# Optimization experiments

Measured on AMD Instinct MI355X. Metric: run time of the kernel, lower is better.

Reference implementation:

```python
import jax, jax.numpy as jnp
import numpy as np

B, T_ENC, ENC_DIM = 32, 200, 256
T_DEC, DEC_OUT = 200, 80
HID = 256
PRENET1, PRENET2 = 256, 128


def _gru_cell(x, h, kernel, rec_kernel, bias):
    # Keras GRUCell, reset_after=True. bias: [2, 3*units] (input bias, recurrent bias)
    xz, xr, xh = jnp.split(x @ kernel + bias[0], 3, axis=-1)
    rz, rr, rh = jnp.split(h @ rec_kernel + bias[1], 3, axis=-1)
    z = jax.nn.sigmoid(xz + rz)
    r = jax.nn.sigmoid(xr + rr)
    hh = jnp.tanh(xh + r * rh)
    return z * h + (1.0 - z) * hh


def setup_inputs() -> dict:
    key = jax.random.key(0)
    ks = jax.random.split(key, 24)
    g = lambda k, shape: (jax.random.normal(k, shape, dtype=jnp.float32) / np.sqrt(shape[0] if len(shape) > 1 else 1.0))
    attn_in = PRENET2 + ENC_DIM  # prenet output concat prev attention
    return {
        "memory": jax.random.normal(ks[0], (B, T_ENC, ENC_DIM), dtype=jnp.float32),
        "dec_inputs": jax.random.normal(ks[1], (B, T_DEC, DEC_OUT), dtype=jnp.float32),
        # Prenet
        "fc1_w": g(ks[2], (DEC_OUT, PRENET1)), "fc1_b": jnp.zeros((PRENET1,), jnp.float32),
        "fc2_w": g(ks[3], (PRENET1, PRENET2)), "fc2_b": jnp.zeros((PRENET2,), jnp.float32),
        # Attention GRU cell
        "attn_k": g(ks[4], (attn_in, 3 * HID)), "attn_rk": g(ks[5], (HID, 3 * HID)),
        "attn_bias": jnp.zeros((2, 3 * HID), jnp.float32),
        # Bahdanau attention
        "W": g(ks[6], (ENC_DIM, ENC_DIM)), "U": g(ks[7], (HID, ENC_DIM)), "V": g(ks[8], (ENC_DIM, 1)),
        # Projection
        "proj_w": g(ks[9], (ENC_DIM + HID, HID)), "proj_b": jnp.zeros((HID,), jnp.float32),
        # Decoder GRU cells
        "rnn1_k": g(ks[10], (HID, 3 * HID)), "rnn1_rk": g(ks[11], (HID, 3 * HID)),
        "rnn1_bias": jnp.zeros((2, 3 * HID), jnp.float32),
        "rnn2_k": g(ks[12], (HID, 3 * HID)), "rnn2_rk": g(ks[13], (HID, 3 * HID)),
        "rnn2_bias": jnp.zeros((2, 3 * HID), jnp.float32),
        # Output projection
        "out_w": g(ks[14], (HID, DEC_OUT)), "out_b": jnp.zeros((DEC_OUT,), jnp.float32),
    }


def reference(memory, dec_inputs, fc1_w, fc1_b, fc2_w, fc2_b, attn_k, attn_rk,
              attn_bias, W, U, V, proj_w, proj_b, rnn1_k, rnn1_rk, rnn1_bias,
              rnn2_k, rnn2_rk, rnn2_bias, out_w, out_b):
    b = memory.shape[0]
    # W(values) is loop-invariant -> precompute (same math as in-step application)
    Wv = memory @ W  # [B, T_enc, ENC_DIM]

    def step(carry, x_t):
        attn, h_a, h1, h2 = carry
        # Prenet (Dropout is identity at inference)
        q = jax.nn.relu(x_t @ fc1_w + fc1_b)
        q = jax.nn.relu(q @ fc2_w + fc2_b)
        # Attention RNN
        h_a = _gru_cell(jnp.concatenate([q, attn], axis=-1), h_a, attn_k, attn_rk, attn_bias)
        # Bahdanau attention
        score = jnp.tanh(Wv + (h_a @ U)[:, None, :]) @ V           # [B, T_enc, 1]
        align = jax.nn.softmax(score, axis=1)                       # [B, T_enc, 1]
        attn = jnp.sum(align * memory, axis=1)                      # [B, ENC_DIM]
        # Projection + 2 decoder GRU cells with residual adds
        proj = jnp.concatenate([attn, h_a], axis=-1) @ proj_w + proj_b
        h1 = _gru_cell(proj, h1, rnn1_k, rnn1_rk, rnn1_bias)
        r1 = proj + h1
        h2 = _gru_cell(r1, h2, rnn2_k, rnn2_rk, rnn2_bias)
        r2 = r1 + h2
        out = r2 @ out_w + out_b
        return (attn, h_a, h1, h2), out

    init = (
        jnp.zeros((b, memory.shape[2]), memory.dtype),  # attention
        jnp.zeros((b, HID), memory.dtype),              # attn rnn state
        jnp.zeros((b, HID), memory.dtype),              # dec rnn1 state
        jnp.zeros((b, HID), memory.dtype),              # dec rnn2 state
    )
    xs = jnp.swapaxes(dec_inputs, 0, 1)  # [T_dec, B, DEC_OUT]
    _, ys = jax.lax.scan(step, init, xs)
    return jnp.swapaxes(ys, 0, 1)  # all_outputs: [B, T_dec, DEC_OUT]
```

## Files before the change

### kernel.cpp

```cpp
#include <hip/hip_runtime.h>
#include <math.h>


#define TENC 200
#define TDEC 200

typedef short bf16x8 __attribute__((ext_vector_type(8)));
typedef float f32x4  __attribute__((ext_vector_type(4)));

#define O_H1B   8192
#define O_H2B   (O_H1B + 16384)
#define O_R1B   (O_H2B + 16384)
#define ZERO_FLOATS (O_R1B + 16384)
#define O_HAS   57344
#define O_UHP   (O_HAS + 200*32*256)
#define O_NP    (O_UHP + 32*32*256)
#define O_ZP    (O_NP + 2*128*256)
#define O_PJ    (O_ZP + 256)
#define O_Q2    (O_PJ + 8192)
#define O_WV    (O_Q2 + 200*32*128)
#define O_R2S   (O_WV + 32*200*256)
#define O_IMG   (O_R2S + 200*32*256)

#define IMGA_OFF  0u
#define IMGC1_OFF 1327104u
#define IMGC2_OFF 1859584u
#define IMGD_OFF  2924544u

__device__ __forceinline__ float sigm(float x)  { return 1.0f / (1.0f + __expf(-x)); }
__device__ __forceinline__ float ftanh(float x) { return 1.0f - 2.0f / (1.0f + __expf(2.0f * x)); }

__device__ __forceinline__ unsigned short f2bf(float f) {
  union { float f; unsigned u; } v; v.f = f;
  return (unsigned short)((v.u + 0x7FFFu + ((v.u >> 16) & 1u)) >> 16);
}
__device__ __forceinline__ float bf2f(unsigned short h) {
  union { unsigned u; float f; } v; v.u = ((unsigned)h) << 16; return v.f;
}

__device__ __forceinline__ void pollwait(const unsigned* p, unsigned tgt, bool act) {
  for (;;) {
    bool ok = true;
    if (act) ok = (__hip_atomic_load(p, __ATOMIC_RELAXED, __HIP_MEMORY_SCOPE_AGENT) >= tgt);
    if (__syncthreads_and((int)ok)) break;
    __builtin_amdgcn_s_sleep(2);
  }
  __builtin_amdgcn_fence(__ATOMIC_ACQUIRE, "agent");
}
__device__ __forceinline__ void set_flag(unsigned* f, unsigned v) {
  __syncthreads();
  if (threadIdx.x == 0) {
    __builtin_amdgcn_fence(__ATOMIC_RELEASE, "agent");
    __hip_atomic_store(f, v, __ATOMIC_RELAXED, __HIP_MEMORY_SCOPE_AGENT);
  }
}

__global__ __launch_bounds__(256) void k_prep(
    const float* __restrict__ aK, const float* __restrict__ aRK,
    const float* __restrict__ Wp,
    const float* __restrict__ K1, const float* __restrict__ RK1,
    const float* __restrict__ K2, const float* __restrict__ RK2,
    unsigned short* __restrict__ img)
{
  int e = blockIdx.x * 256 + threadIdx.x;
  int id = blockIdx.y;
  float w = 0.f; size_t oh = 0, ol = 0;
  if (id == 0) {
    if (e >= 32*32*648) return;
    int k = e % 648, n = (e / 648) & 31, blk = e / (648*32);
    int u = blk*8 + (n & 7), g = n >> 3;
    if (k < 384) {
      w = (g==0) ? aK[(size_t)k*768+u] : (g==1) ? aK[(size_t)k*768+256+u]
        : (g==2) ? aK[(size_t)k*768+512+u] : 0.f;
    } else if (k < 640) {
      int kk = k - 384;
      w = (g==0) ? aRK[(size_t)kk*768+u] : (g==1) ? aRK[(size_t)kk*768+256+u]
        : (g==3) ? aRK[(size_t)kk*768+512+u] : 0.f;
    }
    size_t base = IMGA_OFF + (size_t)blk*2*32*648;
    oh = base + (size_t)n*648 + k; ol = oh + 32*648;
  } else if (id == 1) {
    if (e >= 32*16*520) return;
    int k = e % 520, n = (e / 520) & 15, blk = e / (520*16);
    if (n < 8 && k < 512) w = Wp[(size_t)k*256 + blk*8 + n];
    size_t base = IMGC1_OFF + (size_t)blk*2*16*520;
    oh = base + (size_t)n*520 + k; ol = oh + 16*520;
  } else {
    if (e >= 32*32*520) return;
    int k = e % 520, n = (e / 520) & 31, blk = e / (520*32);
    int u = blk*8 + (n & 7), g = n >> 3;
    const float* Kx = (id == 2) ? K1 : K2;
    const float* Rx = (id == 2) ? RK1 : RK2;
    if (k < 256) {
      w = (g==0) ? Kx[(size_t)k*768+u] : (g==1) ? Kx[(size_t)k*768+256+u]
        : (g==2) ? Kx[(size_t)k*768+512+u] : 0.f;
    } else if (k < 512) {
      int kk = k - 256;
      w = (g==0) ? Rx[(size_t)kk*768+u] : (g==1) ? Rx[(size_t)kk*768+256+u]
        : (g==3) ? Rx[(size_t)kk*768+512+u] : 0.f;
    }
    size_t base = ((id == 2) ? IMGC2_OFF : IMGD_OFF) + (size_t)blk*2*32*520;
    oh = base + (size_t)n*520 + k; ol = oh + 32*520;
  }
  unsigned short hi = f2bf(w);
  unsigned short lo = f2bf(w - bf2f(hi));
  img[oh] = hi; img[ol] = lo;
}

__global__ __launch_bounds__(256, 1) void k_scan6(
    const float* __restrict__ memg,
    const float* __restrict__ aB, const float* __restrict__ Uw,
    const float* __restrict__ Vw, const float* __restrict__ pb,
    const float* __restrict__ B1v, const float* __restrict__ B2v,
    float* __restrict__ ws)
{
  const int tid = threadIdx.x, bid = blockIdx.x;
  const int lane = tid & 63, wv = tid >> 6;
  unsigned* fl = (unsigned*)ws;
  float* fH1B = ws + O_H1B;  float* fH2B = ws + O_H2B;  float* fR1B = ws + O_R1B;
  float* fHAS = ws + O_HAS;  float* fUHP = ws + O_UHP;
  float* fNP  = ws + O_NP;   float* fZP  = ws + O_ZP;   float* fPJ = ws + O_PJ;
  float* fQ2  = ws + O_Q2;   float* fWV  = ws + O_WV;   float* fR2S = ws + O_R2S;
  const unsigned short* img = (const unsigned short*)(ws + O_IMG);

  __shared__ __align__(16) char smem[140544];

  if (bid < 32) {
    const int j = bid;
    unsigned* myflag = fl + (0 + j) * 32;
    unsigned short* sW = (unsigned short*)smem;
    unsigned short* sX = (unsigned short*)(smem + 82944);
    float* sU  = (float*)(smem + 124416);
    float* sOut= (float*)(smem + 132608);
    float* sHN = (float*)(smem + 137216);
    float* sHP = (float*)(smem + 138240);
    float* sB  = (float*)(smem + 139264);
    float* sZi = (float*)(smem + 139392);
    {
      const uint4* src = (const uint4*)(img + IMGA_OFF + (size_t)j*2*32*648);
      uint4* dst = (uint4*)sW;
      for (int i = tid; i < 82944/16; i += 256) dst[i] = src[i];
      for (int i = tid; i < 2048; i += 256)
        sU[i] = Uw[(size_t)(j*8 + (i >> 8))*256 + (i & 255)];
      if (tid < 8) {
        int u = j*8 + tid;
        sB[tid]      = aB[u]       + aB[768 + u];
        sB[8 + tid]  = aB[256 + u] + aB[1024 + u];
        sB[16 + tid] = aB[512 + u];
        sB[24 + tid] = aB[1280 + u];
      }
    }
    __syncthreads();
    for (int t = 0; t < TDEC; ++t) {
      for (int i = tid; i < 4096; i += 256) {
        int b = i >> 7, k = i & 127;
        sX[b*648 + k] = f2bf(fQ2[((size_t)t*32 + b)*128 + k]);
      }
      pollwait(fl + (32 + (tid & 127))*32, (unsigned)t, (t > 0) && (tid < 128));
      if (t > 0 && tid < 32) {
        int p = (t - 1) & 1;
        sZi[tid] = 1.0f / (fZP[p*128 + tid*4] + fZP[p*128 + tid*4 + 1] +
                           fZP[p*128 + tid*4 + 2] + fZP[p*128 + tid*4 + 3]);
      }
      __syncthreads();
      for (int i = tid; i < 8192; i += 256) {
        int b = i >> 8, d = i & 255; float v = 0.f;
        if (t > 0) {
          int p = (t - 1) & 1;
          const float* np = fNP + (size_t)p*32768 + (size_t)(b*4)*256 + d;
          v = (np[0] + np[256] + np[512] + np[768]) * sZi[b];
        }
        sX[b*648 + 128 + d] = f2bf(v);
      }
      for (int i = tid; i < 8192; i += 256) {
        int b = i >> 8, d = i & 255;
        float v = (t > 0) ? fHAS[((size_t)(t-1)*32 + b)*256 + d] : 0.f;
        sX[b*648 + 384 + d] = f2bf(v);
      }
      { int b = tid >> 3, ul = tid & 7;
        sHP[tid] = (t > 0) ? fHAS[((size_t)(t-1)*32 + b)*256 + j*8 + ul] : 0.f; }
      __syncthreads();
      {
        const int mt = wv >> 1, nt = wv & 1;
        f32x4 acc = {0.f, 0.f, 0.f, 0.f};
        const unsigned short* xr = sX + (size_t)(mt*16 + (lane&15))*648 + ((lane>>4)*8);
        const unsigned short* wh = sW + (size_t)(nt*16 + (lane&15))*648 + ((lane>>4)*8);
        const unsigned short* wl = wh + 32*648;
        for (int kt = 0; kt < 20; ++kt) {
          bf16x8 a  = *(const bf16x8*)(xr + kt*32);
          bf16x8 bh = *(const bf16x8*)(wh + kt*32);
          bf16x8 bl = *(const bf16x8*)(wl + kt*32);
          acc = __builtin_amdgcn_mfma_f32_16x16x32_bf16(a, bh, acc, 0, 0, 0);
          acc = __builtin_amdgcn_mfma_f32_16x16x32_bf16(a, bl, acc, 0, 0, 0);
        }
        int r0 = mt*16 + ((lane>>4)<<2), c = nt*16 + (lane&15);
        #pragma unroll
        for (int i2 = 0; i2 < 4; ++i2) sOut[(r0+i2)*36 + c] = acc[i2];
      }
      __syncthreads();
      { int b = tid >> 3, ul = tid & 7;
        float z = sigm(sOut[b*36 + ul] + sB[ul]);
        float r = sigm(sOut[b*36 + 8 + ul] + sB[8+ul]);
        float hh = ftanh(sOut[b*36 + 16 + ul] + sB[16+ul] + r*(sOut[b*36 + 24 + ul] + sB[24+ul]));
        float hn = z * sHP[tid] + (1.0f - z) * hh;
        sHN[tid] = hn;
        fHAS[((size_t)t*32 + b)*256 + j*8 + ul] = hn;
      }
      __syncthreads();
      {
        int dq = tid >> 5, b = tid & 31;
        float h0 = sHN[b*8+0], h1 = sHN[b*8+1], h2 = sHN[b*8+2], h3 = sHN[b*8+3];
        float h4 = sHN[b*8+4], h5 = sHN[b*8+5], h6 = sHN[b*8+6], h7 = sHN[b*8+7];
        float* dst = fUHP + ((size_t)j*32 + b)*256 + dq*32;
        #pragma unroll 4
        for (int dd = 0; dd < 32; ++dd) {
          int d = dq*32 + dd;
          dst[dd] = h0*sU[d] + h1*sU[256+d] + h2*sU[512+d] + h3*sU[768+d]
                  + h4*sU[1024+d] + h5*sU[1280+d] + h6*sU[1536+d] + h7*sU[1792+d];
        }
      }
      set_flag(myflag, (unsigned)(t + 1));
    }
  } else if (bid < 160) {
    const int idx = bid - 32, b = idx >> 2, q = idx & 3;
    unsigned* myflag = fl + (32 + idx) * 32;
    float* sWV  = (float*)smem;
    float* sMem = (float*)(smem + 52000);
    float* sV   = (float*)(smem + 104000);
    float* sUh  = (float*)(smem + 105024);
    float* sE   = (float*)(smem + 106048);
    float* sZ   = (float*)(smem + 106304);
    for (int i = tid; i < 50*256; i += 256) {
      int r = i >> 8, d = i & 255;
      sWV[r*260 + d]  = fWV[((size_t)b*200 + q*50 + r)*256 + d];
      sMem[r*260 + d] = memg[((size_t)b*200 + q*50 + r)*256 + d];
    }
    sV[tid] = Vw[tid];
    __syncthreads();
    for (int t = 0; t < TDEC; ++t) {
      {
        const unsigned* p; unsigned tg; bool act;
        if (tid < 32)      { p = fl + tid*32;               tg = (unsigned)(t+1); act = true; }
        else if (tid < 64) { p = fl + (160 + tid - 32)*32;  tg = (unsigned)t;     act = (t > 0); }
        else               { p = fl;                        tg = 0u;              act = false; }
        pollwait(p, tg, act);
      }
      { float s = 0.f;
        #pragma unroll 4
        for (int j2 = 0; j2 < 32; ++j2) s += fUHP[((size_t)j2*32 + b)*256 + tid];
        sUh[tid] = s; }
      __syncthreads();
      { int r = tid >> 2, qd = tid & 3;
        float part = 0.f;
        if (r < 50) {
          const float* wvp = sWV + r*260 + qd*64;
          const float* uh = sUh + qd*64;
          const float* vv = sV + qd*64;
          #pragma unroll 8
          for (int i2 = 0; i2 < 64; ++i2) part += vv[i2] * ftanh(wvp[i2] + uh[i2]);
        }
        part += __shfl_down(part, 2, 4);
        part += __shfl_down(part, 1, 4);
        if (r < 50 && qd == 0) sE[r] = __expf(part);
      }
      __syncthreads();
      if (tid < 64) {
        float e = (tid < 50) ? sE[tid] : 0.f;
        #pragma unroll
        for (int off = 32; off; off >>= 1) e += __shfl_xor(e, off, 64);
        if (tid == 0) sZ[0] = e;
      }
      __syncthreads();
      { float acc = 0.f;
        #pragma unroll 2
        for (int r = 0; r < 50; ++r) acc += sE[r] * sMem[r*260 + tid];
        fNP[(size_t)(t & 1)*32768 + ((size_t)b*4 + q)*256 + tid] = acc; }
      if (tid == 0) fZP[(t & 1)*128 + b*4 + q] = sZ[0];
      set_flag(myflag, (unsigned)(t + 1));
    }
  } else if (bid < 192) {
    const int j = bid - 160;
    unsigned* flagC1 = fl + (160 + j) * 32;
    unsigned* flagC2 = fl + (192 + j) * 32;
    unsigned short* sW1 = (unsigned short*)smem;
    unsigned short* sW2 = (unsigned short*)(smem + 33280);
    unsigned short* sX  = (unsigned short*)(smem + 99840);
    float* sOut = (float*)(smem + 133120);
    float* sPJ  = (float*)(smem + 137728);
    float* sH1p = (float*)(smem + 138752);
    float* sB   = (float*)(smem + 139776);
    float* sZi  = (float*)(smem + 139968);
    {
      const uint4* s1 = (const uint4*)(img + IMGC1_OFF + (size_t)j*2*16*520);
      uint4* d1 = (uint4*)sW1;
      for (int i = tid; i < 33280/16; i += 256) d1[i] = s1[i];
      const uint4* s2 = (const uint4*)(img + IMGC2_OFF + (size_t)j*2*32*520);
      uint4* d2 = (uint4*)sW2;
      for (int i = tid; i < 66560/16; i += 256) d2[i] = s2[i];
      if (tid < 8) {
        int u = j*8 + tid;
        sB[tid]      = B1v[u]       + B1v[768 + u];
        sB[8 + tid]  = B1v[256 + u] + B1v[1024 + u];
        sB[16 + tid] = B1v[512 + u];
        sB[24 + tid] = B1v[1280 + u];
        sB[32 + tid] = pb[u];
      }
    }
    __syncthreads();
    for (int t = 0; t < TDEC; ++t) {
      {
        const unsigned* p; unsigned tg; bool act;
        if (tid < 128)      { p = fl + (32 + tid)*32;         tg = (unsigned)(t+1); act = true; }
        else if (tid < 160) { p = fl + (192 + tid - 128)*32;  tg = (unsigned)t;     act = (t > 0); }
        else if (tid < 192) { p = fl + (224 + tid - 160)*32;  tg = (unsigned)(t-1); act = (t >= 2); }
        else                { p = fl;                         tg = 0u;              act = false; }
        pollwait(p, tg, act);
      }
      if (tid < 32) {
        int p = t & 1;
        sZi[tid] = 1.0f / (fZP[p*128 + tid*4] + fZP[p*128 + tid*4 + 1] +
                           fZP[p*128 + tid*4 + 2] + fZP[p*128 + tid*4 + 3]);
      }
      __syncthreads();
      for (int i = tid; i < 8192; i += 256) {
        int b = i >> 8, d = i & 255;
        int p = t & 1;
        const float* np = fNP + (size_t)p*32768 + (size_t)(b*4)*256 + d;
        sX[b*520 + d] = f2bf((np[0] + np[256] + np[512] + np[768]) * sZi[b]);
      }
      for (int i = tid; i < 8192; i += 256) {
        int b = i >> 8, d = i & 255;
        sX[b*520 + 256 + d] = f2bf(fHAS[((size_t)t*32 + b)*256 + d]);
      }
      __syncthreads();
      if (wv < 2) {
        const int mt = wv;
        f32x4 acc = {0.f, 0.f, 0.f, 0.f};
        const unsigned short* xr = sX + (size_t)(mt*16 + (lane&15))*520 + ((lane>>4)*8);
        const unsigned short* wh = sW1 + (size_t)(lane&15)*520 + ((lane>>4)*8);
        const unsigned short* wl = wh + 16*520;
        for (int kt = 0; kt < 16; ++kt) {
          bf16x8 a  = *(const bf16x8*)(xr + kt*32);
          bf16x8 bh = *(const bf16x8*)(wh + kt*32);
          bf16x8 bl = *(const bf16x8*)(wl + kt*32);
          acc = __builtin_amdgcn_mfma_f32_16x16x32_bf16(a, bh, acc, 0, 0, 0);
          acc = __builtin_amdgcn_mfma_f32_16x16x32_bf16(a, bl, acc, 0, 0, 0);
        }
        int r0 = mt*16 + ((lane>>4)<<2), c = lane & 15;
        #pragma unroll
        for (int i2 = 0; i2 < 4; ++i2) sOut[(r0+i2)*36 + c] = acc[i2];
      }
      __syncthreads();
      { int b = tid >> 3, ul = tid & 7;
        float pj = sOut[b*36 + ul] + sB[32 + ul];
        sPJ[tid] = pj;
        fPJ[(size_t)b*256 + j*8 + ul] = pj; }
      set_flag(flagC1, (unsigned)(t + 1));
      pollwait(fl + (160 + (tid & 31))*32, (unsigned)(t + 1), tid < 32);
      for (int i = tid; i < 8192; i += 256) {
        int b = i >> 8, d = i & 255;
        sX[b*520 + d] = f2bf(fPJ[(size_t)b*256 + d]);
      }
      for (int i = tid; i < 8192; i += 256) {
        int b = i >> 8, d = i & 255;
        sX[b*520 + 256 + d] = f2bf(fH1B[(size_t)(t & 1)*8192 + (size_t)b*256 + d]);
      }
      { int b = tid >> 3, ul = tid & 7;
        sH1p[tid] = fH1B[(size_t)(t & 1)*8192 + (size_t)b*256 + j*8 + ul]; }
      __syncthreads();
      {
        const int mt = wv >> 1, nt = wv & 1;
        f32x4 acc = {0.f, 0.f, 0.f, 0.f};
        const unsigned short* xr = sX + (size_t)(mt*16 + (lane&15))*520 + ((lane>>4)*8);
        const unsigned short* wh = sW2 + (size_t)(nt*16 + (lane&15))*520 + ((lane>>4)*8);
        const unsigned short* wl = wh + 32*520;
        for (int kt = 0; kt < 16; ++kt) {
          bf16x8 a  = *(const bf16x8*)(xr + kt*32);
          bf16x8 bh = *(const bf16x8*)(wh + kt*32);
          bf16x8 bl = *(const bf16x8*)(wl + kt*32);
          acc = __builtin_amdgcn_mfma_f32_16x16x32_bf16(a, bh, acc, 0, 0, 0);
          acc = __builtin_amdgcn_mfma_f32_16x16x32_bf16(a, bl, acc, 0, 0, 0);
        }
        int r0 = mt*16 + ((lane>>4)<<2), c = nt*16 + (lane&15);
        #pragma unroll
        for (int i2 = 0; i2 < 4; ++i2) sOut[(r0+i2)*36 + c] = acc[i2];
      }
      __syncthreads();
      { int b = tid >> 3, ul = tid & 7;
        float z = sigm(sOut[b*36 + ul] + sB[ul]);
        float r = sigm(sOut[b*36 + 8 + ul] + sB[8+ul]);
        float hh = ftanh(sOut[b*36 + 16 + ul] + sB[16+ul] + r*(sOut[b*36 + 24 + ul] + sB[24+ul]));
        float hn = z * sH1p[tid] + (1.0f - z) * hh;
        fH1B[(size_t)((t+1) & 1)*8192 + (size_t)b*256 + j*8 + ul] = hn;
        fR1B[(size_t)(t & 1)*8192 + (size_t)b*256 + j*8 + ul] = sPJ[tid] + hn;
      }
      set_flag(flagC2, (unsigned)(t + 1));
    }
  } else {
    const int j = bid - 192;
    unsigned* myflag = fl + (224 + j) * 32;
    unsigned short* sW = (unsigned short*)smem;
    unsigned short* sX = (unsigned short*)(smem + 66560);
    float* sOut = (float*)(smem + 99840);
    float* sR1f = (float*)(smem + 104448);
    float* sH2p = (float*)(smem + 105472);
    float* sB   = (float*)(smem + 106496);
    {
      const uint4* s2 = (const uint4*)(img + IMGD_OFF + (size_t)j*2*32*520);
      uint4* d2 = (uint4*)sW;
      for (int i = tid; i < 66560/16; i += 256) d2[i] = s2[i];
      if (tid < 8) {
        int u = j*8 + tid;
        sB[tid]      = B2v[u]       + B2v[768 + u];
        sB[8 + tid]  = B2v[256 + u] + B2v[1024 + u];
        sB[16 + tid] = B2v[512 + u];
        sB[24 + tid] = B2v[1280 + u];
      }
    }
    __syncthreads();
    for (int t = 0; t < TDEC; ++t) {
      {
        const unsigned* p; unsigned tg; bool act;
        if (tid < 32)      { p = fl + (192 + tid)*32;       tg = (unsigned)(t+1); act = true; }
        else if (tid < 64) { p = fl + (224 + tid - 32)*32;  tg = (unsigned)t;     act = (t > 0); }
        else               { p = fl;                        tg = 0u;              act = false; }
        pollwait(p, tg, act);
      }
      for (int i = tid; i < 8192; i += 256) {
        int b = i >> 8, d = i & 255;
        sX[b*520 + d] = f2bf(fR1B[(size_t)(t & 1)*8192 + (size_t)b*256 + d]);
      }
      for (int i = tid; i < 8192; i += 256) {
        int b = i >> 8, d = i & 255;
        sX[b*520 + 256 + d] = f2bf(fH2B[(size_t)(t & 1)*8192 + (size_t)b*256 + d]);
      }
      { int b = tid >> 3, ul = tid & 7;
        sR1f[tid] = fR1B[(size_t)(t & 1)*8192 + (size_t)b*256 + j*8 + ul];
        sH2p[tid] = fH2B[(size_t)(t & 1)*8192 + (size_t)b*256 + j*8 + ul]; }
      __syncthreads();
      { const int mt = wv >> 1, nt = wv & 1;
        f32x4 acc = {0.f, 0.f, 0.f, 0.f};
        const unsigned short* xr = sX + (size_t)(mt*16 + (lane&15))*520 + ((lane>>4)*8);
        const unsigned short* wh = sW + (size_t)(nt*16 + (lane&15))*520 + ((lane>>4)*8);
        const unsigned short* wl = wh + 32*520;
        for (int kt = 0; kt < 16; ++kt) {
          bf16x8 a  = *(const bf16x8*)(xr + kt*32);
          bf16x8 bh = *(const bf16x8*)(wh + kt*32);
          bf16x8 bl = *(const bf16x8*)(wl + kt*32);
          acc = __builtin_amdgcn_mfma_f32_16x16x32_bf16(a, bh, acc, 0, 0, 0);
          acc = __builtin_amdgcn_mfma_f32_16x16x32_bf16(a, bl, acc, 0, 0, 0);
        }
        int r0 = mt*16 + ((lane>>4)<<2), c = nt*16 + (lane&15);
        #pragma unroll
        for (int i2 = 0; i2 < 4; ++i2) sOut[(r0+i2)*36 + c] = acc[i2];
      }
      __syncthreads();
      { int b = tid >> 3, ul = tid & 7;
        float z = sigm(sOut[b*36 + ul] + sB[ul]);
        float r = sigm(sOut[b*36 + 8 + ul] + sB[8+ul]);
        float hh = ftanh(sOut[b*36 + 16 + ul] + sB[16+ul] + r*(sOut[b*36 + 24 + ul] + sB[24+ul]));
        float hn = z * sH2p[tid] + (1.0f - z) * hh;
        fH2B[(size_t)((t+1) & 1)*8192 + (size_t)b*256 + j*8 + ul] = hn;
        fR2S[((size_t)t*32 + b)*256 + j*8 + ul] = sR1f[tid] + hn;
      }
      set_flag(myflag, (unsigned)(t + 1));
    }
  }
}

__global__ __launch_bounds__(256) void k_wv(
    const float* __restrict__ mem, const float* __restrict__ W, float* __restrict__ wv)
{
  const int tile = blockIdx.x, b = blockIdx.y;
  const int t0 = tile * 8, tid = threadIdx.x;
  __shared__ float rows[2048];
  for (int i = tid; i < 2048; i += 256) rows[i] = mem[((size_t)b*TENC + t0)*256 + i];
  __syncthreads();
  float acc[8] = {0,0,0,0,0,0,0,0};
  for (int k = 0; k < 256; ++k) {
    float w = W[(size_t)k*256 + tid];
    #pragma unroll
    for (int tt = 0; tt < 8; ++tt) acc[tt] += rows[tt*256 + k] * w;
  }
  #pragma unroll
  for (int tt = 0; tt < 8; ++tt) wv[((size_t)b*TENC + t0 + tt)*256 + tid] = acc[tt];
}

__global__ __launch_bounds__(256) void k_prenet(
    const float* __restrict__ x, const float* __restrict__ w1, const float* __restrict__ b1,
    const float* __restrict__ w2, const float* __restrict__ b2, float* __restrict__ q2)
{
  const int tile = blockIdx.x, b = blockIdx.y;
  const int t0 = tile * 4, tid = threadIdx.x;
  __shared__ float xr[320];
  __shared__ float q1[1024];
  for (int i = tid; i < 320; i += 256) {
    int tt = i / 80, k = i - tt*80;
    xr[i] = x[((size_t)b*TDEC + t0 + tt)*80 + k];
  }
  __syncthreads();
  {
    float a0 = 0.f, a1 = 0.f, a2 = 0.f, a3 = 0.f;
    for (int k = 0; k < 80; ++k) {
      float w = w1[(size_t)k*256 + tid];
      a0 += xr[k]*w; a1 += xr[80+k]*w; a2 += xr[160+k]*w; a3 += xr[240+k]*w;
    }
    float bb = b1[tid];
    q1[tid]       = fmaxf(a0 + bb, 0.f);
    q1[256 + tid] = fmaxf(a1 + bb, 0.f);
    q1[512 + tid] = fmaxf(a2 + bb, 0.f);
    q1[768 + tid] = fmaxf(a3 + bb, 0.f);
  }
  __syncthreads();
  {
    const int jj = tid & 127, tp = tid >> 7;
    float c0 = 0.f, c1 = 0.f;
    for (int k = 0; k < 256; ++k) {
      float w = w2[(size_t)k*128 + jj];
      c0 += q1[(2*tp)*256 + k] * w;
      c1 += q1[(2*tp + 1)*256 + k] * w;
    }
    float bb = b2[jj];
    q2[(((size_t)t0 + 2*tp)*32 + b)*128 + jj]     = fmaxf(c0 + bb, 0.f);
    q2[(((size_t)t0 + 2*tp + 1)*32 + b)*128 + jj] = fmaxf(c1 + bb, 0.f);
  }
}

__global__ __launch_bounds__(128) void k_out(
    const float* __restrict__ r2, const float* __restrict__ wo,
    const float* __restrict__ bo, float* __restrict__ out)
{
  const int tb = blockIdx.x;
  const int t = tb >> 5, b = tb & 31, tid = threadIdx.x;
  __shared__ float row[256];
  for (int i = tid; i < 256; i += 128) row[i] = r2[(size_t)tb*256 + i];
  __syncthreads();
  if (tid < 80) {
    float acc = bo[tid];
    #pragma unroll 4
    for (int k = 0; k < 256; ++k) acc += row[k] * wo[(size_t)k*80 + tid];
    out[((size_t)b*TDEC + t)*80 + tid] = acc;
  }
}

extern "C" void kernel_launch(void* const* d_in, const int* in_sizes, int n_in,
                              void* d_out, int out_size, void* d_ws, size_t ws_size,
                              hipStream_t stream)
{
  const float* mem = (const float*)d_in[0];
  const float* dec = (const float*)d_in[1];
  const float* w1  = (const float*)d_in[2];
  const float* b1  = (const float*)d_in[3];
  const float* w2  = (const float*)d_in[4];
  const float* b2  = (const float*)d_in[5];
  const float* aK  = (const float*)d_in[6];
  const float* aRK = (const float*)d_in[7];
  const float* aB  = (const float*)d_in[8];
  const float* W   = (const float*)d_in[9];
  const float* U   = (const float*)d_in[10];
  const float* V   = (const float*)d_in[11];
  const float* Wp  = (const float*)d_in[12];
  const float* pb  = (const float*)d_in[13];
  const float* K1  = (const float*)d_in[14];
  const float* RK1 = (const float*)d_in[15];
  const float* B1v = (const float*)d_in[16];
  const float* K2  = (const float*)d_in[17];
  const float* RK2 = (const float*)d_in[18];
  const float* B2v = (const float*)d_in[19];
  const float* Wo  = (const float*)d_in[20];
  const float* bo  = (const float*)d_in[21];
  float* ws  = (float*)d_ws;
  float* out = (float*)d_out;

  hipMemsetAsync(ws, 0, (size_t)ZERO_FLOATS * sizeof(float), stream);
  k_prep<<<dim3(2592, 4), 256, 0, stream>>>(aK, aRK, Wp, K1, RK1, K2, RK2,
                                            (unsigned short*)(ws + O_IMG));
  k_wv<<<dim3(25, 32), 256, 0, stream>>>(mem, W, ws + O_WV);
  k_prenet<<<dim3(50, 32), 256, 0, stream>>>(dec, w1, b1, w2, b2, ws + O_Q2);
  k_scan6<<<224, 256, 0, stream>>>(mem, aB, U, V, pb, B1v, B2v, ws);
  k_out<<<6400, 128, 0, stream>>>(ws + O_R2S, Wo, bo, out);
}
```

Before: 7.125 ms.

## Move U-projection into attention blocks and reduce attention context in leader block

The attention-GRU blocks no longer compute and publish per-slice partial h_a@U products. Each attention block instead waits for the full h_a and computes h_a@U itself from global U. Also, the q=0 attention block per batch gathers the other three partial contexts and softmax sums, normalises them, and publishes a final attention vector plus one flag per batch. Consumers now poll 32 flags instead of 128 and read one reduced vector. This trades redundant 256x256 matvecs per block and an extra serial reduction hop for fewer cross-block flag waits and less reduction traffic on the critical path.

Result: slower. 8.427 ms (+18.3%).

```diff
diff --git a/kernel.cpp b/kernel.cpp
--- a/kernel.cpp
+++ b/kernel.cpp
@@ -8,19 +8,19 @@
 typedef short bf16x8 __attribute__((ext_vector_type(8)));
 typedef float f32x4  __attribute__((ext_vector_type(4)));
 
-#define O_H1B   8192
-#define O_H2B   (O_H1B + 16384)
-#define O_R1B   (O_H2B + 16384)
-#define ZERO_FLOATS (O_R1B + 16384)
-#define O_HAS   57344
-#define O_UHP   (O_HAS + 200*32*256)
-#define O_NP    (O_UHP + 32*32*256)
-#define O_ZP    (O_NP + 2*128*256)
-#define O_PJ    (O_ZP + 256)
-#define O_Q2    (O_PJ + 8192)
-#define O_WV    (O_Q2 + 200*32*128)
-#define O_R2S   (O_WV + 32*200*256)
-#define O_IMG   (O_R2S + 200*32*256)
+#define O_H1B 8192
+#define O_H2B 24576
+#define O_R1B 40960
+#define O_AT  57344
+#define O_NPQ 73728
+#define O_ZPQ 98304
+#define O_PJ  98432
+#define ZERO_FLOATS 106624
+#define O_HAS 106624
+#define O_Q2  (O_HAS + 200*32*256)
+#define O_WV  (O_Q2 + 200*32*128)
+#define O_R2S (O_WV + 32*200*256)
+#define O_IMG (O_R2S + 200*32*256)
 
 #define IMGA_OFF  0u
 #define IMGC1_OFF 1327104u
@@ -107,7 +107,7 @@
   img[oh] = hi; img[ol] = lo;
 }
 
-__global__ __launch_bounds__(256, 1) void k_scan6(
+__global__ __launch_bounds__(256, 1) void k_scan7(
     const float* __restrict__ memg,
     const float* __restrict__ aB, const float* __restrict__ Uw,
     const float* __restrict__ Vw, const float* __restrict__ pb,
@@ -118,8 +118,8 @@
   const int lane = tid & 63, wv = tid >> 6;
   unsigned* fl = (unsigned*)ws;
   float* fH1B = ws + O_H1B;  float* fH2B = ws + O_H2B;  float* fR1B = ws + O_R1B;
-  float* fHAS = ws + O_HAS;  float* fUHP = ws + O_UHP;
-  float* fNP  = ws + O_NP;   float* fZP  = ws + O_ZP;   float* fPJ = ws + O_PJ;
+  float* fAT  = ws + O_AT;   float* fNPq = ws + O_NPQ;  float* fZPq = ws + O_ZPQ;
+  float* fPJ  = ws + O_PJ;   float* fHAS = ws + O_HAS;
   float* fQ2  = ws + O_Q2;   float* fWV  = ws + O_WV;   float* fR2S = ws + O_R2S;
   const unsigned short* img = (const unsigned short*)(ws + O_IMG);
 
@@ -127,21 +127,16 @@
 
   if (bid < 32) {
     const int j = bid;
-    unsigned* myflag = fl + (0 + j) * 32;
+    unsigned* myflag = fl + j * 32;
     unsigned short* sW = (unsigned short*)smem;
     unsigned short* sX = (unsigned short*)(smem + 82944);
-    float* sU  = (float*)(smem + 124416);
-    float* sOut= (float*)(smem + 132608);
-    float* sHN = (float*)(smem + 137216);
-    float* sHP = (float*)(smem + 138240);
-    float* sB  = (float*)(smem + 139264);
-    float* sZi = (float*)(smem + 139392);
+    float* sOut = (float*)(smem + 124416);
+    float* sHP  = (float*)(smem + 129024);
+    float* sB   = (float*)(smem + 130048);
     {
       const uint4* src = (const uint4*)(img + IMGA_OFF + (size_t)j*2*32*648);
       uint4* dst = (uint4*)sW;
       for (int i = tid; i < 82944/16; i += 256) dst[i] = src[i];
-      for (int i = tid; i < 2048; i += 256)
-        sU[i] = Uw[(size_t)(j*8 + (i >> 8))*256 + (i & 255)];
       if (tid < 8) {
         int u = j*8 + tid;
         sB[tid]      = aB[u]       + aB[768 + u];
@@ -156,20 +151,11 @@
         int b = i >> 7, k = i & 127;
         sX[b*648 + k] = f2bf(fQ2[((size_t)t*32 + b)*128 + k]);
       }
-      pollwait(fl + (32 + (tid & 127))*32, (unsigned)t, (t > 0) && (tid < 128));
-      if (t > 0 && tid < 32) {
-        int p = (t - 1) & 1;
-        sZi[tid] = 1.0f / (fZP[p*128 + tid*4] + fZP[p*128 + tid*4 + 1] +
-                           fZP[p*128 + tid*4 + 2] + fZP[p*128 + tid*4 + 3]);
-      }
-      __syncthreads();
-      for (int i = tid; i < 8192; i += 256) {
-        int b = i >> 8, d = i & 255; float v = 0.f;
-        if (t > 0) {
-          int p = (t - 1) & 1;
-          const float* np = fNP + (size_t)p*32768 + (size_t)(b*4)*256 + d;
-          v = (np[0] + np[256] + np[512] + np[768]) * sZi[b];
-        }
+      pollwait(fl + (128 + (tid & 31))*32, (unsigned)t, (t > 0) && (tid < 32));
+      const float* at = fAT + (size_t)((t-1) & 1)*8192;
+      for (int i = tid; i < 8192; i += 256) {
+        int b = i >> 8, d = i & 255;
+        float v = (t > 0) ? at[b*256 + d] : 0.f;
         sX[b*648 + 128 + d] = f2bf(v);
       }
       for (int i = tid; i < 8192; i += 256) {
@@ -203,33 +189,22 @@
         float r = sigm(sOut[b*36 + 8 + ul] + sB[8+ul]);
         float hh = ftanh(sOut[b*36 + 16 + ul] + sB[16+ul] + r*(sOut[b*36 + 24 + ul] + sB[24+ul]));
         float hn = z * sHP[tid] + (1.0f - z) * hh;
-        sHN[tid] = hn;
         fHAS[((size_t)t*32 + b)*256 + j*8 + ul] = hn;
-      }
-      __syncthreads();
-      {
-        int dq = tid >> 5, b = tid & 31;
-        float h0 = sHN[b*8+0], h1 = sHN[b*8+1], h2 = sHN[b*8+2], h3 = sHN[b*8+3];
-        float h4 = sHN[b*8+4], h5 = sHN[b*8+5], h6 = sHN[b*8+6], h7 = sHN[b*8+7];
-        float* dst = fUHP + ((size_t)j*32 + b)*256 + dq*32;
-        #pragma unroll 4
-        for (int dd = 0; dd < 32; ++dd) {
-          int d = dq*32 + dd;
-          dst[dd] = h0*sU[d] + h1*sU[256+d] + h2*sU[512+d] + h3*sU[768+d]
-                  + h4*sU[1024+d] + h5*sU[1280+d] + h6*sU[1536+d] + h7*sU[1792+d];
-        }
       }
       set_flag(myflag, (unsigned)(t + 1));
     }
   } else if (bid < 160) {
     const int idx = bid - 32, b = idx >> 2, q = idx & 3;
-    unsigned* myflag = fl + (32 + idx) * 32;
+    unsigned* myflag = fl + (32 + b*3 + (q - 1)) * 32;
     float* sWV  = (float*)smem;
     float* sMem = (float*)(smem + 52000);
     float* sV   = (float*)(smem + 104000);
-    float* sUh  = (float*)(smem + 105024);
-    float* sE   = (float*)(smem + 106048);
-    float* sZ   = (float*)(smem + 106304);
+    float* sHA  = (float*)(smem + 105024);
+    float* sUh  = (float*)(smem + 106048);
+    float* sE   = (float*)(smem + 107072);
+    float* sZ   = (float*)(smem + 107328);
+    float* sCtx = (float*)(smem + 107392);
+    float* sZs  = (float*)(smem + 108416);
     for (int i = tid; i < 50*256; i += 256) {
       int r = i >> 8, d = i & 255;
       sWV[r*260 + d]  = fWV[((size_t)b*200 + q*50 + r)*256 + d];
@@ -238,17 +213,14 @@
     sV[tid] = Vw[tid];
     __syncthreads();
     for (int t = 0; t < TDEC; ++t) {
+      pollwait(fl + (tid & 31)*32, (unsigned)(t + 1), tid < 32);
+      sHA[tid] = fHAS[((size_t)t*32 + b)*256 + tid];
+      __syncthreads();
       {
-        const unsigned* p; unsigned tg; bool act;
-        if (tid < 32)      { p = fl + tid*32;               tg = (unsigned)(t+1); act = true; }
-        else if (tid < 64) { p = fl + (160 + tid - 32)*32;  tg = (unsigned)t;     act = (t > 0); }
-        else               { p = fl;                        tg = 0u;              act = false; }
-        pollwait(p, tg, act);
-      }
-      { float s = 0.f;
-        #pragma unroll 4
-        for (int j2 = 0; j2 < 32; ++j2) s += fUHP[((size_t)j2*32 + b)*256 + tid];
-        sUh[tid] = s; }
+        float acc = 0.f;
+        #pragma unroll 8
+        for (int k = 0; k < 256; ++k) acc += sHA[k] * Uw[(size_t)k*256 + tid];
+        sUh[tid] = acc; }
       __syncthreads();
       { int r = tid >> 2, qd = tid & 3;
         float part = 0.f;
@@ -274,9 +246,27 @@
       { float acc = 0.f;
         #pragma unroll 2
         for (int r = 0; r < 50; ++r) acc += sE[r] * sMem[r*260 + tid];
-        fNP[(size_t)(t & 1)*32768 + ((size_t)b*4 + q)*256 + tid] = acc; }
-      if (tid == 0) fZP[(t & 1)*128 + b*4 + q] = sZ[0];
-      set_flag(myflag, (unsigned)(t + 1));
+        if (q) fNPq[((size_t)b*3 + q - 1)*256 + tid] = acc;
+        else   sCtx[tid] = acc; }
+      if (q) {
+        if (tid == 0) fZPq[b*3 + q - 1] = sZ[0];
+        set_flag(myflag, (unsigned)(t + 1));
+      } else {
+        { const unsigned* p; unsigned tg; bool act;
+          if (tid < 3)                    { p = fl + (32 + b*3 + tid)*32; tg = (unsigned)(t+1); act = true; }
+          else if (tid >= 32 && tid < 64) { p = fl + (160 + tid - 32)*32; tg = (unsigned)(t-1); act = (t >= 2); }
+          else                            { p = fl;                       tg = 0u;              act = false; }
+          pollwait(p, tg, act);
+        }
+        if (tid < 3) sZs[tid] = fZPq[b*3 + tid];
+        __syncthreads();
+        float Zi = 1.0f / (sZ[0] + sZs[0] + sZs[1] + sZs[2]);
+        float av = (sCtx[tid] + fNPq[(size_t)(b*3 + 0)*256 + tid]
+                             + fNPq[(size_t)(b*3 + 1)*256 + tid]
+                             + fNPq[(size_t)(b*3 + 2)*256 + tid]) * Zi;
+        fAT[(size_t)(t & 1)*8192 + b*256 + tid] = av;
+        set_flag(fl + (128 + b)*32, (unsigned)(t + 1));
+      }
     }
   } else if (bid < 192) {
     const int j = bid - 160;
@@ -289,7 +279,6 @@
     float* sPJ  = (float*)(smem + 137728);
     float* sH1p = (float*)(smem + 138752);
     float* sB   = (float*)(smem + 139776);
-    float* sZi  = (float*)(smem + 139968);
     {
       const uint4* s1 = (const uint4*)(img + IMGC1_OFF + (size_t)j*2*16*520);
       uint4* d1 = (uint4*)sW1;
@@ -310,23 +299,16 @@
     for (int t = 0; t < TDEC; ++t) {
       {
         const unsigned* p; unsigned tg; bool act;
-        if (tid < 128)      { p = fl + (32 + tid)*32;         tg = (unsigned)(t+1); act = true; }
-        else if (tid < 160) { p = fl + (192 + tid - 128)*32;  tg = (unsigned)t;     act = (t > 0); }
-        else if (tid < 192) { p = fl + (224 + tid - 160)*32;  tg = (unsigned)(t-1); act = (t >= 2); }
-        else                { p = fl;                         tg = 0u;              act = false; }
+        if (tid < 32)      { p = fl + (128 + tid)*32;       tg = (unsigned)(t+1); act = true; }
+        else if (tid < 64) { p = fl + (192 + tid - 32)*32;  tg = (unsigned)t;     act = (t > 0); }
+        else if (tid < 96) { p = fl + (224 + tid - 64)*32;  tg = (unsigned)(t-1); act = (t >= 2); }
+        else               { p = fl;                        tg = 0u;              act = false; }
         pollwait(p, tg, act);
       }
-      if (tid < 32) {
-        int p = t & 1;
-        sZi[tid] = 1.0f / (fZP[p*128 + tid*4] + fZP[p*128 + tid*4 + 1] +
-                           fZP[p*128 + tid*4 + 2] + fZP[p*128 + tid*4 + 3]);
-      }
-      __syncthreads();
-      for (int i = tid; i < 8192; i += 256) {
-        int b = i >> 8, d = i & 255;
-        int p = t & 1;
-        const float* np = fNP + (size_t)p*32768 + (size_t)(b*4)*256 + d;
-        sX[b*520 + d] = f2bf((np[0] + np[256] + np[512] + np[768]) * sZi[b]);
+      const float* at = fAT + (size_t)(t & 1)*8192;
+      for (int i = tid; i < 8192; i += 256) {
+        int b = i >> 8, d = i & 255;
+        sX[b*520 + d] = f2bf(at[b*256 + d]);
       }
       for (int i = tid; i < 8192; i += 256) {
         int b = i >> 8, d = i & 255;
@@ -419,8 +401,7 @@
     }
     __syncthreads();
     for (int t = 0; t < TDEC; ++t) {
-      {
-        const unsigned* p; unsigned tg; bool act;
+      { const unsigned* p; unsigned tg; bool act;
         if (tid < 32)      { p = fl + (192 + tid)*32;       tg = (unsigned)(t+1); act = true; }
         else if (tid < 64) { p = fl + (224 + tid - 32)*32;  tg = (unsigned)t;     act = (t > 0); }
         else               { p = fl;                        tg = 0u;              act = false; }
@@ -577,6 +558,6 @@
                                             (unsigned short*)(ws + O_IMG));
   k_wv<<<dim3(25, 32), 256, 0, stream>>>(mem, W, ws + O_WV);
   k_prenet<<<dim3(50, 32), 256, 0, stream>>>(dec, w1, b1, w2, b2, ws + O_Q2);
-  k_scan6<<<224, 256, 0, stream>>>(mem, aB, U, V, pb, B1v, B2v, ws);
+  k_scan7<<<224, 256, 0, stream>>>(mem, aB, U, V, pb, B1v, B2v, ws);
   k_out<<<6400, 128, 0, stream>>>(ws + O_R2S, Wo, bo, out);
 }
```
